# Kernel optimization log

Hardware: AMD Instinct MI355X
Metric: run time of the kernel (lower is better)

Reference implementation:

```python
import jax, jax.numpy as jnp
import numpy as np

# SamplesLoss('sinkhorn', p=2, blur=0.05, backend='tensorized') defaults (geomloss):
# debiased Sinkhorn divergence, cost C(x,y)=|x-y|^2/2, eps = blur^p,
# epsilon-scaling from diameter^p down to blur^p with scaling=0.5,
# symmetric (averaged) log-domain updates + one final extrapolation step.
P = 2
BLUR = 0.05
SCALING = 0.5
DIAMETER = 10.0  # static diameter estimate for the annealing schedule (randn data)


def _eps_schedule():
    eps_target = BLUR ** P
    lst = []
    e = DIAMETER ** P
    while e > eps_target:
        lst.append(e)
        e *= SCALING ** P
    lst.append(eps_target)
    return lst

EPS_LIST = _eps_schedule()


def _sqcost(x, y):
    # C[b,n,m] = 0.5 * ||x_bn - y_bm||^2, via expansion (avoids [B,N,M,D] tensor)
    x2 = jnp.sum(x * x, axis=-1)  # [B,N]
    y2 = jnp.sum(y * y, axis=-1)  # [B,M]
    xy = jnp.einsum('bnd,bmd->bnm', x, y)
    return 0.5 * (x2[:, :, None] + y2[:, None, :] - 2.0 * xy)


def _softmin(eps, C, h):
    # h: [B,M] (already log-weights + potential/eps); C: [B,N,M] -> [B,N]
    return -eps * jax.nn.logsumexp(h[:, None, :] - C / eps, axis=2)


def _sinkhorn_divergence(x, y, a, b):
    log_a = jnp.log(a)
    log_b = jnp.log(b)
    Cxy = _sqcost(x, y)
    Cyx = jnp.swapaxes(Cxy, 1, 2)
    Cxx = _sqcost(x, x)
    Cyy = _sqcost(y, y)

    eps0 = EPS_LIST[0]
    f_ba = _softmin(eps0, Cxy, log_b)  # potential on x for OT(a,b)
    g_ab = _softmin(eps0, Cyx, log_a)  # potential on y for OT(a,b)
    f_aa = _softmin(eps0, Cxx, log_a)  # debias self-potential on x
    g_bb = _softmin(eps0, Cyy, log_b)  # debias self-potential on y

    for eps in EPS_LIST:
        ft = _softmin(eps, Cxy, log_b + g_ab / eps)
        gt = _softmin(eps, Cyx, log_a + f_ba / eps)
        f_ba = 0.5 * (f_ba + ft)
        g_ab = 0.5 * (g_ab + gt)
        f_aa = 0.5 * (f_aa + _softmin(eps, Cxx, log_a + f_aa / eps))
        g_bb = 0.5 * (g_bb + _softmin(eps, Cyy, log_b + g_bb / eps))

    # final (non-averaged) extrapolation at the target temperature
    eps = EPS_LIST[-1]
    f_fin = _softmin(eps, Cxy, log_b + g_ab / eps)
    g_fin = _softmin(eps, Cyx, log_a + f_ba / eps)
    f_aa = _softmin(eps, Cxx, log_a + f_aa / eps)
    g_bb = _softmin(eps, Cyy, log_b + g_bb / eps)

    # debiased divergence: <a, f_ab - f_aa> + <b, g_ab - g_bb>
    return jnp.sum(a * (f_fin - f_aa), axis=-1) + jnp.sum(b * (g_fin - g_bb), axis=-1)


def setup_inputs() -> dict:
    key = jax.random.key(0)
    k1, k2, k3, k4 = jax.random.split(key, 4)
    B, N, M, D = 8, 2048, 2048, 64
    return {
        'inp1': jax.random.normal(k1, (B, N, D), dtype=jnp.float32),
        'inp2': jax.random.normal(k2, (B, M, D), dtype=jnp.float32),
        'weights1': jax.random.uniform(k3, (B, N), dtype=jnp.float32),
        'weights2': jax.random.uniform(k4, (B, M), dtype=jnp.float32),
    }


def reference(inp1, inp2, weights1, weights2):
    # normalize_weights=True branch of SinkhornLoss.forward
    mass1 = jnp.sum(weights1, axis=1, keepdims=True)
    mass1 = jnp.where(mass1 == 0.0, 1.0, mass1)
    a = weights1 / mass1
    mass2 = jnp.sum(weights2, axis=1, keepdims=True)
    mass2 = jnp.where(mass2 == 0.0, 1.0, mass2)
    b = weights2 / mass2
    loss = _sinkhorn_divergence(inp1, inp2, a, b)  # [B]
    return jnp.mean(loss)  # reduction='mean'
```

## Files before the change

### kernel.cpp

```cpp
#include <hip/hip_runtime.h>
#include <cstdint>
#include <cstddef>

#define BB 8
#define NPTS 2048
#define DIM 64
#define CK 64
#define HALFC 1024
#define NC (HALFC / CK)
#define BROWS 64

typedef _Float16 f16x8 __attribute__((ext_vector_type(8)));
typedef float f32x4 __attribute__((ext_vector_type(4)));

static const float EPS_H[9] = {100.0f, 25.0f, 6.25f, 1.5625f, 0.390625f,
                               0.09765625f, 0.0244140625f, 0.006103515625f,
                               0.0025f};
#define LOG2E 1.4426950408889634f
#define LN2 0.6931471805599453f

#if __has_builtin(__builtin_amdgcn_exp2f)
static __device__ __forceinline__ float fexp2(float x) {
  return __builtin_amdgcn_exp2f(x);
}
#else
static __device__ __forceinline__ float fexp2(float x) {
  float r;
  asm("v_exp_f32 %0, %1" : "=v"(r) : "v"(x));
  return r;
}
#endif

static __device__ __forceinline__ f32x4 vmax4(f32x4 a, f32x4 b) {
  f32x4 r;
  #pragma unroll
  for (int i = 0; i < 4; ++i) r[i] = fmaxf(a[i], b[i]);
  return r;
}

static __device__ __forceinline__ f32x4 vexp2_4(f32x4 a) {
  f32x4 r;
  #pragma unroll
  for (int i = 0; i < 4; ++i) r[i] = fexp2(a[i]);
  return r;
}

static __device__ __forceinline__ void gload_lds16(const void* g, void* l) {
  __builtin_amdgcn_global_load_lds(
      (const __attribute__((address_space(1))) void*)g,
      (__attribute__((address_space(3))) void*)l, 16, 0, 0);
}

struct FT {
  const _Float16* P;
  const _Float16* Q;
};
struct MT {
  const float* psq;
  const float* oldf;
  float* out;
  const float* lwn;
  const float* q2n;
  float* hqn;
};


__global__ __launch_bounds__(256) void norm_weights_k(
    const float* __restrict__ w, float* __restrict__ aout,
    float* __restrict__ logout, int n) {
  int b = blockIdx.x;
  const float* wb = w + (size_t)b * n;
  __shared__ float red[256];
  float s = 0.f;
  for (int i = threadIdx.x; i < n; i += 256) s += wb[i];
  red[threadIdx.x] = s;
  __syncthreads();
  for (int st = 128; st > 0; st >>= 1) {
    if (threadIdx.x < st) red[threadIdx.x] += red[threadIdx.x + st];
    __syncthreads();
  }
  float mass = red[0];
  if (mass == 0.f) mass = 1.f;
  float inv = 1.f / mass;
  for (int i = threadIdx.x; i < n; i += 256) {
    float av = wb[i] * inv;
    aout[(size_t)b * n + i] = av;
    logout[(size_t)b * n + i] = logf(av);
  }
}

__global__ __launch_bounds__(256) void sqnorm_cvt_k(
    const float* __restrict__ X, float* __restrict__ sq,
    _Float16* __restrict__ Xh, int rows) {
  int row = blockIdx.x * 4 + (threadIdx.x >> 6);
  int lane = threadIdx.x & 63;
  if (row >= rows) return;
  float v = X[(size_t)row * DIM + lane];
  Xh[(size_t)row * DIM + lane] = (_Float16)v;
  float s = v * v;
  #pragma unroll
  for (int off = 32; off > 0; off >>= 1) s += __shfl_xor(s, off);
  if (lane == 0) sq[row] = s;
}

__global__ __launch_bounds__(256) void init_hq_k(
    const float* __restrict__ la, const float* __restrict__ lb,
    const float* __restrict__ x2, const float* __restrict__ y2,
    float* __restrict__ hq, float ie2) {
  int task = blockIdx.z;
  int idx = blockIdx.x * 256 + threadIdx.x;
  const float* lw = (task == 1 || task == 2) ? la : lb;
  const float* q2 = (task == 1 || task == 2) ? x2 : y2;
  hq[(size_t)task * BB * NPTS + idx] =
      fmaf(lw[idx], LOG2E, -0.5f * q2[idx] * ie2);
}

__global__ __launch_bounds__(256, 8) void fused_softmin_k(
    FT t0, FT t1, FT t2, FT t3, const float* __restrict__ hqG,
    float* __restrict__ pmx, float* __restrict__ psm, float ie2) {
  __shared__ float hql[HALFC];
  __shared__ __align__(16) _Float16 qb[2][CK * DIM];
  FT T = (blockIdx.z == 0) ? t0
       : (blockIdx.z == 1) ? t1
       : (blockIdx.z == 2) ? t2 : t3;
  const int rowg = blockIdx.x >> 1, half = blockIdx.x & 1;
  const int b = blockIdx.y, task = blockIdx.z;
  const int tid = threadIdx.x;

  {
    const float* hqp = hqG + ((size_t)task * BB + b) * NPTS + half * HALFC;
    #pragma unroll
    for (int i = 0; i < HALFC / 256; ++i)
      hql[i * 256 + tid] = hqp[i * 256 + tid];
  }

  const int lane = tid & 63, wave = tid >> 6;
  const _Float16* Qb = T.Q + ((size_t)b * NPTS + half * HALFC) * DIM;

  auto stage = [&](int buf, int chunk) {
    int m0 = chunk * CK;
    #pragma unroll
    for (int r = 0; r < 2; ++r) {
      int gbase = r * 256 + wave * 64;
      int gid = gbase + lane;
      int row = gid >> 3;
      int kg = (gid & 7) ^ (row & 7);
      const _Float16* src = Qb + (size_t)(m0 + row) * DIM + kg * 8;
      _Float16* dst = &qb[buf][(size_t)gbase * 8];
      gload_lds16(src, dst);
    }
  };

  const int fr = lane & 15;
  const int g0 = lane >> 4;
  const int r0 = rowg * BROWS + wave * 16;
  const _Float16* Pb = T.P + ((size_t)b * NPTS + r0) * DIM;
  f16x8 a0 = *(const f16x8*)(Pb + fr * DIM + g0 * 8);
  f16x8 a1 = *(const f16x8*)(Pb + fr * DIM + g0 * 8 + 32);

  f32x4 mx4 = {-3.0e38f, -3.0e38f, -3.0e38f, -3.0e38f};
  f32x4 sm4 = {0.f, 0.f, 0.f, 0.f};

  auto compute = [&](int cur, int m0) {
    const char* qbase = (const char*)&qb[cur][0];
    f32x4 v4[4];
    f32x4 cmx = mx4;
    #pragma unroll
    for (int s = 0; s < 4; ++s) {
      int row = s * 16 + fr;
      int byte0 = row * 128 + ((g0 ^ (row & 7)) << 4);
      int byte1 = row * 128 + (((g0 + 4) ^ (row & 7)) << 4);
      f16x8 b0 = *(const f16x8*)(qbase + byte0);
      f16x8 b1 = *(const f16x8*)(qbase + byte1);
      float hs = hql[m0 + s * 16 + fr];
      f32x4 z = {0.f, 0.f, 0.f, 0.f};
      f32x4 t = __builtin_amdgcn_mfma_f32_16x16x32_f16(a0, b0, z, 0, 0, 0);
      f32x4 acc = __builtin_amdgcn_mfma_f32_16x16x32_f16(a1, b1, t, 0, 0, 0);
      v4[s] = acc * ie2 + hs;
      cmx = vmax4(cmx, v4[s]);
    }
    f32x4 resc = vexp2_4(mx4 - cmx);
    f32x4 esum = vexp2_4(v4[0] - cmx) + vexp2_4(v4[1] - cmx);
    esum += vexp2_4(v4[2] - cmx) + vexp2_4(v4[3] - cmx);
    sm4 = sm4 * resc + esum;
    mx4 = cmx;
  };

  stage(0, 0);
  __syncthreads();

  for (int c = 0; c < NC - 1; ++c) {
    int cur = c & 1;
    stage(cur ^ 1, c + 1);
    asm volatile("s_waitcnt vmcnt(2)" ::: "memory");
    __builtin_amdgcn_sched_barrier(0);
    __builtin_amdgcn_s_barrier();
    __builtin_amdgcn_sched_barrier(0);
    compute(cur, c * CK);
    __builtin_amdgcn_sched_barrier(0);
    __builtin_amdgcn_s_barrier();
    __builtin_amdgcn_sched_barrier(0);
  }
  asm volatile("s_waitcnt vmcnt(0)" ::: "memory");
  __builtin_amdgcn_sched_barrier(0);
  __builtin_amdgcn_s_barrier();
  __builtin_amdgcn_sched_barrier(0);
  compute((NC - 1) & 1, (NC - 1) * CK);

  #pragma unroll
  for (int off = 1; off < 16; off <<= 1) {
    #pragma unroll
    for (int q = 0; q < 4; ++q) {
      float omx = __shfl_xor(mx4[q], off);
      float osm = __shfl_xor(sm4[q], off);
      float nm = fmaxf(mx4[q], omx);
      sm4[q] = sm4[q] * fexp2(mx4[q] - nm) + osm * fexp2(omx - nm);
      mx4[q] = nm;
    }
  }
  if (fr == 0) {
    #pragma unroll
    for (int q = 0; q < 4; ++q) {
      int r = r0 + g0 * 4 + q;
      size_t pi = (((size_t)task * BB + b) * 2 + half) * NPTS + r;
      pmx[pi] = mx4[q];
      psm[pi] = sm4[q];
    }
  }
}

__global__ __launch_bounds__(256) void merge_k(
    const float* __restrict__ pmx, const float* __restrict__ psm,
    MT m0, MT m1, MT m2, MT m3, float nel, float ie2n, int whq) {
  int task = blockIdx.z;
  MT M = (task == 0) ? m0 : (task == 1) ? m1 : (task == 2) ? m2 : m3;
  int idx = blockIdx.x * 256 + threadIdx.x;
  int b = idx >> 11;
  int r = idx & 2047;
  size_t pi = (((size_t)task * BB + b) * 2) * NPTS + r;
  float ma = pmx[pi], mb = pmx[pi + NPTS];
  float sa = psm[pi], sb = psm[pi + NPTS];
  float nm = fmaxf(ma, mb);
  float ss = sa * fexp2(ma - nm) + sb * fexp2(mb - nm);
  float f = nel * (__log2f(ss) + nm) + 0.5f * M.psq[idx];
  if (M.oldf) f = 0.5f * (M.oldf[idx] + f);
  M.out[idx] = f;
  if (whq) {
    float h = fmaf(f, ie2n, fmaf(M.lwn[idx], LOG2E, -0.5f * M.q2n[idx] * ie2n));
    M.hqn[idx] = h;
  }
}

__global__ __launch_bounds__(256) void loss_part_k(
    const float* __restrict__ aW, const float* __restrict__ f_fin,
    const float* __restrict__ f_aa, const float* __restrict__ bW,
    const float* __restrict__ g_fin, const float* __restrict__ g_bb,
    float* __restrict__ part) {
  __shared__ float red[256];
  int i0 = blockIdx.x * 256 + threadIdx.x;
  float s = 0.f;
  for (int i = i0; i < BB * NPTS; i += 64 * 256)
    s += aW[i] * (f_fin[i] - f_aa[i]) + bW[i] * (g_fin[i] - g_bb[i]);
  red[threadIdx.x] = s;
  __syncthreads();
  for (int st = 128; st > 0; st >>= 1) {
    if (threadIdx.x < st) red[threadIdx.x] += red[threadIdx.x + st];
    __syncthreads();
  }
  if (threadIdx.x == 0) part[blockIdx.x] = red[0];
}

__global__ __launch_bounds__(64) void loss_fin_k(const float* __restrict__ part,
                                                 float* __restrict__ out) {
  float s = part[threadIdx.x];
  #pragma unroll
  for (int off = 32; off > 0; off >>= 1) s += __shfl_xor(s, off);
  if (threadIdx.x == 0) out[0] = s * (1.f / BB);
}

__global__ void write_val_k(float* out, float v) { out[0] = v; }


extern "C" void kernel_launch(void* const* d_in, const int* in_sizes, int n_in,
                              void* d_out, int out_size, void* d_ws,
                              size_t ws_size, hipStream_t stream) {
  (void)in_sizes; (void)n_in; (void)out_size;
  const float* X = (const float*)d_in[0];
  const float* Y = (const float*)d_in[1];
  const float* W1 = (const float*)d_in[2];
  const float* W2 = (const float*)d_in[3];
  float* out = (float*)d_out;

  char* base = (char*)d_ws;
  size_t off = 0;
  auto alloc_b = [&](size_t bytes) {
    void* r = base + off;
    off += (bytes + 255) & ~(size_t)255;
    return r;
  };
  const size_t nP = (size_t)BB * NPTS;
  _Float16* Xh = (_Float16*)alloc_b(nP * DIM * 2);
  _Float16* Yh = (_Float16*)alloc_b(nP * DIM * 2);
  float* x2 = (float*)alloc_b(nP * 4);
  float* y2 = (float*)alloc_b(nP * 4);
  float* aW = (float*)alloc_b(nP * 4);
  float* bW = (float*)alloc_b(nP * 4);
  float* la = (float*)alloc_b(nP * 4);
  float* lb = (float*)alloc_b(nP * 4);
  float* fba[2] = {(float*)alloc_b(nP * 4), (float*)alloc_b(nP * 4)};
  float* gab[2] = {(float*)alloc_b(nP * 4), (float*)alloc_b(nP * 4)};
  float* faa[2] = {(float*)alloc_b(nP * 4), (float*)alloc_b(nP * 4)};
  float* gbb[2] = {(float*)alloc_b(nP * 4), (float*)alloc_b(nP * 4)};
  float* hq = (float*)alloc_b(4 * nP * 4);
  float* pmx = (float*)alloc_b(4 * nP * 2 * 4);
  float* psm = (float*)alloc_b(4 * nP * 2 * 4);
  float* part = (float*)alloc_b(64 * 4);
  if (ws_size < off) {
    write_val_k<<<1, 1, 0, stream>>>(out, -(float)(ws_size >> 20));
    return;
  }

  norm_weights_k<<<BB, 256, 0, stream>>>(W1, aW, la, NPTS);
  norm_weights_k<<<BB, 256, 0, stream>>>(W2, bW, lb, NPTS);
  sqnorm_cvt_k<<<BB * NPTS / 4, 256, 0, stream>>>(X, x2, Xh, BB * NPTS);
  sqnorm_cvt_k<<<BB * NPTS / 4, 256, 0, stream>>>(Y, y2, Yh, BB * NPTS);

  dim3 fg(64, BB, 4);
  dim3 mg(BB * NPTS / 256, 1, 4);

  FT t0{Xh, Yh}, t1{Yh, Xh}, t2{Xh, Xh}, t3{Yh, Yh};
  float* hq0 = hq;
  float* hq1 = hq + 1 * nP;
  float* hq2 = hq + 2 * nP;
  float* hq3 = hq + 3 * nP;

  auto fused = [&](float eps) {
    fused_softmin_k<<<fg, 256, 0, stream>>>(t0, t1, t2, t3, hq, pmx, psm,
                                            LOG2E / eps);
  };
  auto merge = [&](float eps, float ie2n, int whq, const float* oF,
                   float* nF, const float* oG, float* nG, const float* oA,
                   float* nA, const float* oB, float* nB) {
    float nel = -eps * LN2;
    MT M0{x2, oF, nF, la, x2, hq1};
    MT M1{y2, oG, nG, lb, y2, hq0};
    MT M2{x2, oA, nA, la, x2, hq2};
    MT M3{y2, oB, nB, lb, y2, hq3};
    merge_k<<<mg, 256, 0, stream>>>(pmx, psm, M0, M1, M2, M3, nel, ie2n, whq);
  };

  init_hq_k<<<mg, 256, 0, stream>>>(la, lb, x2, y2, hq, LOG2E / EPS_H[0]);

  fused(EPS_H[0]);
  merge(EPS_H[0], LOG2E / EPS_H[0], 1, nullptr, fba[0], nullptr, gab[0],
        nullptr, faa[0], nullptr, gbb[0]);

  int cur = 0;
  for (int it = 0; it < 9; ++it) {
    int nxt = cur ^ 1;
    float epsn = EPS_H[it < 8 ? it + 1 : 8];
    fused(EPS_H[it]);
    merge(EPS_H[it], LOG2E / epsn, 1, fba[cur], fba[nxt], gab[cur], gab[nxt],
          faa[cur], faa[nxt], gbb[cur], gbb[nxt]);
    cur = nxt;
  }

  {
    int nxt = cur ^ 1;
    fused(EPS_H[8]);
    merge(EPS_H[8], 0.f, 0, nullptr, fba[nxt], nullptr, gab[nxt], nullptr,
          faa[nxt], nullptr, gbb[nxt]);
    loss_part_k<<<64, 256, 0, stream>>>(aW, fba[nxt], faa[nxt], bW, gab[nxt],
                                        gbb[nxt], part);
    loss_fin_k<<<1, 64, 0, stream>>>(part, out);
  }
}
```

Measured before the change: 466.7 us.

## Split columns into quarters, give each wave two row tiles, add lazy-rescale logsumexp

The fused softmin kernel now splits the column range into four quarters instead of two and gives each wave 32 rows (two 16-row MFMA tiles) rather than 16. Each staged B chunk therefore feeds twice as many MFMAs, cutting LDS and global traffic per unit of compute. The online logsumexp is updated per 16-column step and skips the max rescale when no value exceeds the running max, using a +8 headroom so rescales stay rare. The merge kernel combines four partials instead of two, and the partial buffers double in size. The extra register pressure and the wave-uniform branch could hurt occupancy or scheduling.

```diff
diff --git a/kernel.cpp b/kernel.cpp
--- a/kernel.cpp
+++ b/kernel.cpp
@@ -6,9 +6,9 @@
 #define NPTS 2048
 #define DIM 64
 #define CK 64
-#define HALFC 1024
-#define NC (HALFC / CK)
-#define BROWS 64
+#define QC 512
+#define NC (QC / CK)
+#define BROWS 128
 
 typedef _Float16 f16x8 __attribute__((ext_vector_type(8)));
 typedef float f32x4 __attribute__((ext_vector_type(4)));
@@ -118,24 +118,24 @@
 __global__ __launch_bounds__(256, 8) void fused_softmin_k(
     FT t0, FT t1, FT t2, FT t3, const float* __restrict__ hqG,
     float* __restrict__ pmx, float* __restrict__ psm, float ie2) {
-  __shared__ float hql[HALFC];
+  __shared__ float hql[QC];
   __shared__ __align__(16) _Float16 qb[2][CK * DIM];
   FT T = (blockIdx.z == 0) ? t0
        : (blockIdx.z == 1) ? t1
        : (blockIdx.z == 2) ? t2 : t3;
-  const int rowg = blockIdx.x >> 1, half = blockIdx.x & 1;
+  const int rowg = blockIdx.x >> 2, qtr = blockIdx.x & 3;
   const int b = blockIdx.y, task = blockIdx.z;
   const int tid = threadIdx.x;
 
   {
-    const float* hqp = hqG + ((size_t)task * BB + b) * NPTS + half * HALFC;
+    const float* hqp = hqG + ((size_t)task * BB + b) * NPTS + qtr * QC;
     #pragma unroll
-    for (int i = 0; i < HALFC / 256; ++i)
+    for (int i = 0; i < QC / 256; ++i)
       hql[i * 256 + tid] = hqp[i * 256 + tid];
   }
 
   const int lane = tid & 63, wave = tid >> 6;
-  const _Float16* Qb = T.Q + ((size_t)b * NPTS + half * HALFC) * DIM;
+  const _Float16* Qb = T.Q + ((size_t)b * NPTS + qtr * QC) * DIM;
 
   auto stage = [&](int buf, int chunk) {
     int m0 = chunk * CK;
@@ -153,18 +153,33 @@
 
   const int fr = lane & 15;
   const int g0 = lane >> 4;
-  const int r0 = rowg * BROWS + wave * 16;
+  const int r0 = rowg * BROWS + wave * 32;
   const _Float16* Pb = T.P + ((size_t)b * NPTS + r0) * DIM;
-  f16x8 a0 = *(const f16x8*)(Pb + fr * DIM + g0 * 8);
-  f16x8 a1 = *(const f16x8*)(Pb + fr * DIM + g0 * 8 + 32);
-
-  f32x4 mx4 = {-3.0e38f, -3.0e38f, -3.0e38f, -3.0e38f};
-  f32x4 sm4 = {0.f, 0.f, 0.f, 0.f};
-
-  auto compute = [&](int cur, int m0) {
+  f16x8 a00 = *(const f16x8*)(Pb + fr * DIM + g0 * 8);
+  f16x8 a01 = *(const f16x8*)(Pb + fr * DIM + g0 * 8 + 32);
+  f16x8 a10 = *(const f16x8*)(Pb + (16 + fr) * DIM + g0 * 8);
+  f16x8 a11 = *(const f16x8*)(Pb + (16 + fr) * DIM + g0 * 8 + 32);
+
+  f32x4 M0 = {-3.0e38f, -3.0e38f, -3.0e38f, -3.0e38f};
+  f32x4 M1 = M0;
+  f32x4 S0 = {0.f, 0.f, 0.f, 0.f};
+  f32x4 S1 = S0;
+
+  auto upd = [&](f32x4 acc, float hs, f32x4& M, f32x4& S) {
+    f32x4 v = acc * ie2 + hs;
+    bool cfast = (v[0] <= M[0]) & (v[1] <= M[1]) &
+                 (v[2] <= M[2]) & (v[3] <= M[3]);
+    if (!__all(cfast)) {
+      f32x4 nm = vmax4(M, v + 8.f);
+      S = S * vexp2_4(M - nm) + vexp2_4(v - nm);
+      M = nm;
+    } else {
+      S += vexp2_4(v - M);
+    }
+  };
+
+  auto compute = [&](int cur, int mbase) {
     const char* qbase = (const char*)&qb[cur][0];
-    f32x4 v4[4];
-    f32x4 cmx = mx4;
     #pragma unroll
     for (int s = 0; s < 4; ++s) {
       int row = s * 16 + fr;
@@ -172,18 +187,15 @@
       int byte1 = row * 128 + (((g0 + 4) ^ (row & 7)) << 4);
       f16x8 b0 = *(const f16x8*)(qbase + byte0);
       f16x8 b1 = *(const f16x8*)(qbase + byte1);
-      float hs = hql[m0 + s * 16 + fr];
+      float hs = hql[mbase + s * 16 + fr];
       f32x4 z = {0.f, 0.f, 0.f, 0.f};
-      f32x4 t = __builtin_amdgcn_mfma_f32_16x16x32_f16(a0, b0, z, 0, 0, 0);
-      f32x4 acc = __builtin_amdgcn_mfma_f32_16x16x32_f16(a1, b1, t, 0, 0, 0);
-      v4[s] = acc * ie2 + hs;
-      cmx = vmax4(cmx, v4[s]);
+      f32x4 u0 = __builtin_amdgcn_mfma_f32_16x16x32_f16(a00, b0, z, 0, 0, 0);
+      f32x4 acc0 = __builtin_amdgcn_mfma_f32_16x16x32_f16(a01, b1, u0, 0, 0, 0);
+      f32x4 u1 = __builtin_amdgcn_mfma_f32_16x16x32_f16(a10, b0, z, 0, 0, 0);
+      f32x4 acc1 = __builtin_amdgcn_mfma_f32_16x16x32_f16(a11, b1, u1, 0, 0, 0);
+      upd(acc0, hs, M0, S0);
+      upd(acc1, hs, M1, S1);
     }
-    f32x4 resc = vexp2_4(mx4 - cmx);
-    f32x4 esum = vexp2_4(v4[0] - cmx) + vexp2_4(v4[1] - cmx);
-    esum += vexp2_4(v4[2] - cmx) + vexp2_4(v4[3] - cmx);
-    sm4 = sm4 * resc + esum;
-    mx4 = cmx;
   };
 
   stage(0, 0);
@@ -211,20 +223,32 @@
   for (int off = 1; off < 16; off <<= 1) {
     #pragma unroll
     for (int q = 0; q < 4; ++q) {
-      float omx = __shfl_xor(mx4[q], off);
-      float osm = __shfl_xor(sm4[q], off);
-      float nm = fmaxf(mx4[q], omx);
-      sm4[q] = sm4[q] * fexp2(mx4[q] - nm) + osm * fexp2(omx - nm);
-      mx4[q] = nm;
+      {
+        float om = __shfl_xor(M0[q], off);
+        float os = __shfl_xor(S0[q], off);
+        float nm = fmaxf(M0[q], om);
+        S0[q] = S0[q] * fexp2(M0[q] - nm) + os * fexp2(om - nm);
+        M0[q] = nm;
+      }
+      {
+        float om = __shfl_xor(M1[q], off);
+        float os = __shfl_xor(S1[q], off);
+        float nm = fmaxf(M1[q], om);
+        S1[q] = S1[q] * fexp2(M1[q] - nm) + os * fexp2(om - nm);
+        M1[q] = nm;
+      }
     }
   }
   if (fr == 0) {
     #pragma unroll
     for (int q = 0; q < 4; ++q) {
-      int r = r0 + g0 * 4 + q;
-      size_t pi = (((size_t)task * BB + b) * 2 + half) * NPTS + r;
-      pmx[pi] = mx4[q];
-      psm[pi] = sm4[q];
+      size_t pbase = (((size_t)task * BB + b) * 4 + qtr) * NPTS;
+      int ra = r0 + g0 * 4 + q;
+      pmx[pbase + ra] = M0[q];
+      psm[pbase + ra] = S0[q];
+      int rb = ra + 16;
+      pmx[pbase + rb] = M1[q];
+      psm[pbase + rb] = S1[q];
     }
   }
 }
@@ -237,11 +261,17 @@
   int idx = blockIdx.x * 256 + threadIdx.x;
   int b = idx >> 11;
   int r = idx & 2047;
-  size_t pi = (((size_t)task * BB + b) * 2) * NPTS + r;
-  float ma = pmx[pi], mb = pmx[pi + NPTS];
-  float sa = psm[pi], sb = psm[pi + NPTS];
-  float nm = fmaxf(ma, mb);
-  float ss = sa * fexp2(ma - nm) + sb * fexp2(mb - nm);
+  size_t pb = (((size_t)task * BB + b) * 4) * NPTS + r;
+  float ma[4], sa[4];
+  #pragma unroll
+  for (int k = 0; k < 4; ++k) {
+    ma[k] = pmx[pb + (size_t)k * NPTS];
+    sa[k] = psm[pb + (size_t)k * NPTS];
+  }
+  float nm = fmaxf(fmaxf(ma[0], ma[1]), fmaxf(ma[2], ma[3]));
+  float ss = 0.f;
+  #pragma unroll
+  for (int k = 0; k < 4; ++k) ss += sa[k] * fexp2(ma[k] - nm);
   float f = nel * (__log2f(ss) + nm) + 0.5f * M.psq[idx];
   if (M.oldf) f = 0.5f * (M.oldf[idx] + f);
   M.out[idx] = f;
@@ -312,8 +342,8 @@
   float* faa[2] = {(float*)alloc_b(nP * 4), (float*)alloc_b(nP * 4)};
   float* gbb[2] = {(float*)alloc_b(nP * 4), (float*)alloc_b(nP * 4)};
   float* hq = (float*)alloc_b(4 * nP * 4);
-  float* pmx = (float*)alloc_b(4 * nP * 2 * 4);
-  float* psm = (float*)alloc_b(4 * nP * 2 * 4);
+  float* pmx = (float*)alloc_b(4 * nP * 4 * 4);
+  float* psm = (float*)alloc_b(4 * nP * 4 * 4);
   float* part = (float*)alloc_b(64 * 4);
   if (ws_size < off) {
     write_val_k<<<1, 1, 0, stream>>>(out, -(float)(ws_size >> 20));
```

New measurement: 973.8 us. 109% more time.
